# Performance work log

Hardware: AMD Instinct MI355X
Metric: run time of the kernel (lower is better)

## Reference

```python
import jax, jax.numpy as jnp
import numpy as np

EMBED_DIM = 2048
NUM_HEADS = 16
HEAD_DIM = EMBED_DIM // NUM_HEADS
WINDOW = 512          # sliding window size (inclusive: q - kv <= WINDOW)
CHUNK = WINDOW        # query chunk size; kv span per chunk = 2*CHUNK
SCALE = 1.0 / float(np.sqrt(HEAD_DIM))


def setup_inputs() -> dict:
    key = jax.random.key(0)
    k1, k2, k3 = jax.random.split(key, 3)
    B, S, E = 2, 4096, EMBED_DIM
    x = jax.random.normal(k1, (B, S, E), dtype=jnp.float32)
    # Linear weights, torch layout [out_features, in_features], small init for stability
    w_qkv = jax.random.normal(k2, (3 * E, E), dtype=jnp.float32) * (1.0 / np.sqrt(E))
    w_out = jax.random.normal(k3, (E, E), dtype=jnp.float32) * (1.0 / np.sqrt(E))
    return {"x": x, "w_qkv": w_qkv, "w_out": w_out}


def _sliding_window_attention(q, k, v):
    # q,k,v: [B,H,S,D]; causal + sliding-window (q_idx - kv_idx in [0, WINDOW])
    B, H, S, D = q.shape
    C = CHUNK
    nc = S // C
    qc = q.reshape(B, H, nc, C, D)                              # [B,H,nc,C,D]
    # pad one zero chunk in front of K/V so each query chunk sees (prev, cur)
    kp = jnp.pad(k, ((0, 0), (0, 0), (C, 0), (0, 0))).reshape(B, H, nc + 1, C, D)
    vp = jnp.pad(v, ((0, 0), (0, 0), (C, 0), (0, 0))).reshape(B, H, nc + 1, C, D)
    kc = jnp.concatenate([kp[:, :, :-1], kp[:, :, 1:]], axis=-2)  # [B,H,nc,2C,D]
    vc = jnp.concatenate([vp[:, :, :-1], vp[:, :, 1:]], axis=-2)  # [B,H,nc,2C,D]

    qa = jnp.arange(C)
    ka = jnp.arange(2 * C)
    diff = C + qa[:, None] - ka[None, :]                        # q_pos - kv_pos, [C,2C]
    base = (diff >= 0) & (diff <= WINDOW)                       # causal + window
    # mask out the zero-padding keys of the first chunk (global kv pos < 0)
    kv_pos = (jnp.arange(nc)[:, None] - 1) * C + ka[None, :]    # [nc,2C]
    mask = base[None, :, :] & (kv_pos >= 0)[:, None, :]         # [nc,C,2C]

    scores = jnp.einsum('bhncd,bhnkd->bhnck', qc, kc) * SCALE   # [B,H,nc,C,2C]
    scores = jnp.where(mask[None, None], scores, -jnp.inf)
    attn = jax.nn.softmax(scores, axis=-1)
    out = jnp.einsum('bhnck,bhnkd->bhncd', attn, vc)            # [B,H,nc,C,D]
    return out.reshape(B, H, S, D)


def reference(x, w_qkv, w_out):
    B, S, E = x.shape
    H, D = NUM_HEADS, HEAD_DIM
    qkv = x @ w_qkv.T                                           # [B,S,3E]
    qkv = qkv.reshape(B, S, 3, H, D).transpose(2, 0, 3, 1, 4)   # [3,B,H,S,D]
    q, k, v = qkv[0], qkv[1], qkv[2]
    o = _sliding_window_attention(q, k, v)                      # [B,H,S,D]
    o = o.transpose(0, 2, 1, 3).reshape(B, S, E)
    return o @ w_out.T
```

## Files before the change

### kernel.cpp

```cpp
#include <hip/hip_runtime.h>


typedef __bf16 bf16x8 __attribute__((ext_vector_type(8)));
typedef float  f32x4  __attribute__((ext_vector_type(4)));
typedef unsigned short u16x4 __attribute__((ext_vector_type(4)));

#define MFMA(a, b, c) __builtin_amdgcn_mfma_f32_16x16x32_bf16(a, b, c, 0, 0, 0)

__device__ __forceinline__ unsigned short f2bf(float f) {
  union { float f; unsigned u; } v; v.f = f;
  unsigned r = v.u + 0x7FFFu + ((v.u >> 16) & 1u);
  return (unsigned short)(r >> 16);
}

__device__ __forceinline__ void gl16(const void* g, void* l) {
  __builtin_amdgcn_global_load_lds(
      (const __attribute__((address_space(1))) unsigned int*)g,
      (__attribute__((address_space(3))) unsigned int*)l, 16, 0, 0);
}

__global__ void cast_bf16(const float4* __restrict__ in,
                          u16x4* __restrict__ out, int n4) {
  int i = blockIdx.x * blockDim.x + threadIdx.x;
  if (i < n4) {
    float4 v = in[i];
    u16x4 o;
    o[0] = f2bf(v.x); o[1] = f2bf(v.y); o[2] = f2bf(v.z); o[3] = f2bf(v.w);
    out[i] = o;
  }
}

template <int MODE>
__global__ __launch_bounds__(512, 2) void gemm_bt(
    const unsigned short* __restrict__ A, const unsigned short* __restrict__ Bw,
    void* __restrict__ C1, void* __restrict__ C2, int K, int Nstride) {
  __shared__ __align__(16) unsigned char sm[131072];
  const int tid = threadIdx.x, lane = tid & 63, w = tid >> 6;
  const int l15 = lane & 15, lg = lane >> 4;
  const int wr = w >> 2, wc = w & 3;

  int id = (int)blockIdx.x;
  int cpx = (int)gridDim.x >> 3;
  int sid = (id & 7) * cpx + (id >> 3);
  const int bm = (sid & 31) * 256;
  const int bn = (sid >> 5) * 256;

  f32x4 acc[8][4] = {};
  const int nt = K >> 6;

  const unsigned short* aRow0 = A  + (size_t)(bm + w * 16 + l15) * K + lg * 8;
  const unsigned short* aRow1 = A  + (size_t)(bm + (w + 8) * 16 + l15) * K + lg * 8;
  const unsigned short* bRow0 = Bw + (size_t)(bn + w * 16 + l15) * K + lg * 8;
  const unsigned short* bRow1 = Bw + (size_t)(bn + (w + 8) * 16 + l15) * K + lg * 8;

  auto stageA = [&](int t, int kk) {
    int kt = ((t < nt) ? t : nt - 1) * 64 + kk * 32;
    unsigned char* dst = sm + (t & 1) * 65536 + kk * 16384;
    gl16(aRow0 + kt, dst + w * 1024);
    gl16(aRow1 + kt, dst + (w + 8) * 1024);
  };
  auto stageB = [&](int t, int kk) {
    int kt = ((t < nt) ? t : nt - 1) * 64 + kk * 32;
    unsigned char* dst = sm + (t & 1) * 65536 + 32768 + kk * 16384;
    gl16(bRow0 + kt, dst + w * 1024);
    gl16(bRow1 + kt, dst + (w + 8) * 1024);
  };

  stageA(0, 0); stageB(0, 0);
  stageA(0, 1); stageB(0, 1);
  stageA(1, 0); stageB(1, 0);
  asm volatile("s_waitcnt vmcnt(8)" ::: "memory");
  __builtin_amdgcn_s_barrier();

#define PHASE(mh, kk, STAGE_STMT, DO_VM, READ_B)                               \
  {                                                                            \
    STAGE_STMT;                                                                \
    bf16x8 af[4];                                                              \
    _Pragma("unroll") for (int i = 0; i < 4; i++)                              \
      af[i] = *(const bf16x8*)(cur + ((kk)*16 + wr * 8 + (mh)*4 + i) * 1024 +  \
                               lane * 16);                                     \
    if (READ_B) {                                                              \
      _Pragma("unroll") for (int j = 0; j < 4; j++)                            \
        bfr[j] = *(const bf16x8*)(cur + 32768 +                                \
                                  ((kk)*16 + wc * 4 + j) * 1024 + lane * 16);  \
    }                                                                          \
    if (DO_VM) asm volatile("s_waitcnt vmcnt(8)" ::: "memory");                \
    __builtin_amdgcn_s_barrier();                                              \
    asm volatile("s_waitcnt lgkmcnt(0)" ::: "memory");                         \
    __builtin_amdgcn_sched_barrier(0);                                         \
    __builtin_amdgcn_s_setprio(1);                                             \
    _Pragma("unroll") for (int i = 0; i < 4; i++)                              \
      _Pragma("unroll") for (int j = 0; j < 4; j++)                            \
        acc[(mh)*4 + i][j] = MFMA(af[i], bfr[j], acc[(mh)*4 + i][j]);          \
    __builtin_amdgcn_s_setprio(0);                                             \
  }

  for (int g = 0; g < nt; ++g) {
    unsigned char* cur = sm + (g & 1) * 65536;
    bf16x8 bfr[4];
    PHASE(0, 0, , false, true)
    PHASE(1, 0, { stageA(g + 1, 1); stageB(g + 1, 1); }, true, false)
    PHASE(0, 1, , false, true)
    PHASE(1, 1, { stageA(g + 2, 0); stageB(g + 2, 0); }, true, false)
  }
#undef PHASE

  asm volatile("s_waitcnt vmcnt(0)" ::: "memory");

  if (MODE == 1) {
    unsigned short* QK = (unsigned short*)C1;
    unsigned short* VT = (unsigned short*)C2;
    if (bn < 4096) {
      const float scl = (bn < 2048) ? 0.08838834764831845f : 1.0f;
#pragma unroll
      for (int mi = 0; mi < 8; mi++) {
        int m0 = bm + wr * 128 + mi * 16 + lg * 4;
#pragma unroll
        for (int j = 0; j < 4; j++) {
          int n = bn + wc * 64 + j * 16 + l15;
#pragma unroll
          for (int r = 0; r < 4; r++)
            QK[(size_t)(m0 + r) * 4096 + n] = f2bf(acc[mi][j][r] * scl);
        }
      }
    } else {
#pragma unroll
      for (int mi = 0; mi < 8; mi++) {
        int m0 = bm + wr * 128 + mi * 16 + lg * 4;
        int bb = m0 >> 12, s = m0 & 4095;
#pragma unroll
        for (int j = 0; j < 4; j++) {
          int n4 = bn + wc * 64 + j * 16 + l15 - 4096;
          int hh = n4 >> 7, d = n4 & 127;
          u16x4 pk;
#pragma unroll
          for (int r = 0; r < 4; r++) pk[r] = f2bf(acc[mi][j][r]);
          *(u16x4*)(VT + ((size_t)((bb * 16 + hh) * 128 + d) * 4096 + s)) = pk;
        }
      }
    }
  } else {
    float* C = (float*)C1;
#pragma unroll
    for (int mi = 0; mi < 8; mi++) {
      int m0 = bm + wr * 128 + mi * 16 + lg * 4;
#pragma unroll
      for (int j = 0; j < 4; j++) {
        int n = bn + wc * 64 + j * 16 + l15;
#pragma unroll
        for (int r = 0; r < 4; r++)
          C[(size_t)(m0 + r) * Nstride + n] = acc[mi][j][r];
      }
    }
  }
}

__global__ __launch_bounds__(256, 2) void attn(
    const unsigned short* __restrict__ QK,
    const unsigned short* __restrict__ VT,
    unsigned short* __restrict__ O) {
  __shared__ unsigned char sm[51200];
  const int tid = threadIdx.x, lane = tid & 63, w = tid >> 6;
  const int l15 = lane & 15, lg = lane >> 4;
  const int bid = blockIdx.x;
  const int sid = (bid & 7) * 128 + (bid >> 3);
  const int qc = sid & 31, h = (sid >> 5) & 15, b = sid >> 9;
  const int q0 = qc * 128;

  bf16x8 qf[2][4];
#pragma unroll
  for (int mb = 0; mb < 2; mb++) {
    const unsigned short* qrow =
        QK + (size_t)(b * 4096 + q0 + (2 * w + mb) * 16 + l15) * 4096 + h * 128 + lg * 8;
#pragma unroll
    for (int ks = 0; ks < 4; ks++) qf[mb][ks] = *(const bf16x8*)(qrow + ks * 32);
  }

  float mrun[2] = {-1e30f, -1e30f}, lrun[2] = {0.f, 0.f};
  f32x4 oacc[8][2] = {};

  const int t0 = (q0 < 512) ? (512 - q0) >> 6 : 0;
  unsigned char* Ps = sm + 32768 + w * 4608;

  for (int t = t0; t < 10; t++) {
    const int kv0 = q0 - 512 + t * 64;
    __syncthreads();
#pragma unroll
    for (int u = 0; u < 4; u++) {
      int f = w + u * 4;
      int kvb = f >> 2, ks = f & 3;
      gl16(QK + (size_t)(b * 4096 + kv0 + kvb * 16 + l15) * 4096 + 2048 + h * 128 + ks * 32 + lg * 8,
           sm + (kvb * 4 + ks) * 1024);
      int db = f >> 1, kvs = f & 1;
      gl16(VT + (size_t)((b * 16 + h) * 128 + db * 16 + l15) * 4096 + kv0 + kvs * 32 + lg * 8,
           sm + 16384 + (db * 2 + kvs) * 1024);
    }
    __syncthreads();

    f32x4 sacc[4][2] = {};
#pragma unroll
    for (int ks = 0; ks < 4; ks++)
#pragma unroll
      for (int kvb = 0; kvb < 4; kvb++) {
        bf16x8 kf = *(const bf16x8*)(sm + (kvb * 4 + ks) * 1024 + lane * 16);
        sacc[kvb][0] = MFMA(kf, qf[0][ks], sacc[kvb][0]);
        sacc[kvb][1] = MFMA(kf, qf[1][ks], sacc[kvb][1]);
      }

    if (t <= 1 || t >= 8) {
#pragma unroll
      for (int kvb = 0; kvb < 4; kvb++)
#pragma unroll
        for (int mb = 0; mb < 2; mb++) {
          int qg = q0 + w * 32 + mb * 16 + l15;
          int kgb = kv0 + kvb * 16 + lg * 4;
#pragma unroll
          for (int r = 0; r < 4; r++) {
            int diff = qg - (kgb + r);
            if (diff < 0 || diff > 512) sacc[kvb][mb][r] = -1e30f;
          }
        }
    }

#pragma unroll
    for (int mb = 0; mb < 2; mb++) {
      float tmax = -1e30f;
#pragma unroll
      for (int kvb = 0; kvb < 4; kvb++)
#pragma unroll
        for (int r = 0; r < 4; r++) tmax = fmaxf(tmax, sacc[kvb][mb][r]);
      tmax = fmaxf(tmax, __shfl_xor(tmax, 16));
      tmax = fmaxf(tmax, __shfl_xor(tmax, 32));
      float mnew = fmaxf(mrun[mb], tmax);
      float alpha = __expf(mrun[mb] - mnew);
      mrun[mb] = mnew;
      float lsum = 0.f;
#pragma unroll
      for (int kvb = 0; kvb < 4; kvb++) {
        u16x4 pk;
#pragma unroll
        for (int r = 0; r < 4; r++) {
          float p = __expf(sacc[kvb][mb][r] - mnew);
          lsum += p;
          pk[r] = f2bf(p);
        }
        *(u16x4*)(Ps + (mb * 16 + l15) * 144 + kvb * 32 + lg * 8) = pk;
      }
      lsum += __shfl_xor(lsum, 16);
      lsum += __shfl_xor(lsum, 32);
      lrun[mb] = lrun[mb] * alpha + lsum;
#pragma unroll
      for (int db = 0; db < 8; db++)
#pragma unroll
        for (int r = 0; r < 4; r++) oacc[db][mb][r] *= alpha;
    }

#pragma unroll
    for (int kvs = 0; kvs < 2; kvs++) {
      bf16x8 pf0 = *(const bf16x8*)(Ps + (0 + l15) * 144 + kvs * 64 + lg * 16);
      bf16x8 pf1 = *(const bf16x8*)(Ps + (16 + l15) * 144 + kvs * 64 + lg * 16);
#pragma unroll
      for (int db = 0; db < 8; db++) {
        bf16x8 vf = *(const bf16x8*)(sm + 16384 + (db * 2 + kvs) * 1024 + lane * 16);
        oacc[db][0] = MFMA(vf, pf0, oacc[db][0]);
        oacc[db][1] = MFMA(vf, pf1, oacc[db][1]);
      }
    }
  }

#pragma unroll
  for (int mb = 0; mb < 2; mb++) {
    float inv = 1.0f / lrun[mb];
    int s = q0 + w * 32 + mb * 16 + l15;
    unsigned short* orow = O + (size_t)(b * 4096 + s) * 2048 + h * 128 + lg * 4;
#pragma unroll
    for (int db = 0; db < 8; db++) {
      u16x4 pk;
#pragma unroll
      for (int r = 0; r < 4; r++) pk[r] = f2bf(oacc[db][mb][r] * inv);
      *(u16x4*)(orow + db * 16) = pk;
    }
  }
}

extern "C" void kernel_launch(void* const* d_in, const int* in_sizes, int n_in,
                              void* d_out, int out_size, void* d_ws, size_t ws_size,
                              hipStream_t stream) {
  const float* x = (const float*)d_in[0];
  const float* w_qkv = (const float*)d_in[1];
  const float* w_out = (const float*)d_in[2];
  float* out = (float*)d_out;

  char* ws = (char*)d_ws;
  unsigned short* XB    = (unsigned short*)(ws);
  unsigned short* WQKVB = (unsigned short*)(ws + 33554432);
  unsigned short* WOUTB = (unsigned short*)(ws + 58720256);
  unsigned short* QKb   = (unsigned short*)(ws + 67108864);
  unsigned short* VTb   = (unsigned short*)(ws + 134217728);
  unsigned short* OB    = XB;

  cast_bf16<<<16384, 256, 0, stream>>>((const float4*)x, (u16x4*)XB, 4194304);
  cast_bf16<<<12288, 256, 0, stream>>>((const float4*)w_qkv, (u16x4*)WQKVB, 3145728);
  cast_bf16<<<4096, 256, 0, stream>>>((const float4*)w_out, (u16x4*)WOUTB, 1048576);

  gemm_bt<1><<<768, 512, 0, stream>>>(XB, WQKVB, QKb, VTb, 2048, 0);

  attn<<<1024, 256, 0, stream>>>(QKb, VTb, OB);

  gemm_bt<2><<<256, 512, 0, stream>>>(OB, WOUTB, out, nullptr, 2048, 2048);
}
```

Measured before the change: 536.1 us.

## Restructure GEMM to 4-stage K32 pipeline and prefetch K/V in attention

The GEMM main loop moves from a two-buffer, K=64 tile with four phases to a four-slot ring of K=32 tiles, issuing one stage per iteration three steps ahead. The attention kernel double-buffers the K tile and prefetches the next K and V tiles while the current tile is computed, replacing the two __syncthreads per iteration with vmcnt waits and barriers. Both changes aim to hide global-to-LDS load latency behind MFMA work. The cost is more LDS in attention (66 KB), which may limit occupancy, and more fine-grained barriers in the GEMM.

Result: no change. 527.7 us (-1.6%).

```diff
diff --git a/kernel.cpp b/kernel.cpp
--- a/kernel.cpp
+++ b/kernel.cpp
@@ -46,64 +46,61 @@
   const int bn = (sid >> 5) * 256;
 
   f32x4 acc[8][4] = {};
-  const int nt = K >> 6;
+  const int nt = K >> 5;
 
   const unsigned short* aRow0 = A  + (size_t)(bm + w * 16 + l15) * K + lg * 8;
   const unsigned short* aRow1 = A  + (size_t)(bm + (w + 8) * 16 + l15) * K + lg * 8;
   const unsigned short* bRow0 = Bw + (size_t)(bn + w * 16 + l15) * K + lg * 8;
   const unsigned short* bRow1 = Bw + (size_t)(bn + (w + 8) * 16 + l15) * K + lg * 8;
 
-  auto stageA = [&](int t, int kk) {
-    int kt = ((t < nt) ? t : nt - 1) * 64 + kk * 32;
-    unsigned char* dst = sm + (t & 1) * 65536 + kk * 16384;
+  auto stage = [&](int t) {
+    int kt = ((t < nt) ? t : nt - 1) * 32;
+    unsigned char* dst = sm + (t & 3) * 32768;
     gl16(aRow0 + kt, dst + w * 1024);
     gl16(aRow1 + kt, dst + (w + 8) * 1024);
+    gl16(bRow0 + kt, dst + 16384 + w * 1024);
+    gl16(bRow1 + kt, dst + 16384 + (w + 8) * 1024);
   };
-  auto stageB = [&](int t, int kk) {
-    int kt = ((t < nt) ? t : nt - 1) * 64 + kk * 32;
-    unsigned char* dst = sm + (t & 1) * 65536 + 32768 + kk * 16384;
-    gl16(bRow0 + kt, dst + w * 1024);
-    gl16(bRow1 + kt, dst + (w + 8) * 1024);
-  };
-
-  stageA(0, 0); stageB(0, 0);
-  stageA(0, 1); stageB(0, 1);
-  stageA(1, 0); stageB(1, 0);
+
+  stage(0); stage(1); stage(2);
   asm volatile("s_waitcnt vmcnt(8)" ::: "memory");
   __builtin_amdgcn_s_barrier();
 
-#define PHASE(mh, kk, STAGE_STMT, DO_VM, READ_B)                               \
-  {                                                                            \
-    STAGE_STMT;                                                                \
-    bf16x8 af[4];                                                              \
-    _Pragma("unroll") for (int i = 0; i < 4; i++)                              \
-      af[i] = *(const bf16x8*)(cur + ((kk)*16 + wr * 8 + (mh)*4 + i) * 1024 +  \
-                               lane * 16);                                     \
-    if (READ_B) {                                                              \
-      _Pragma("unroll") for (int j = 0; j < 4; j++)                            \
-        bfr[j] = *(const bf16x8*)(cur + 32768 +                                \
-                                  ((kk)*16 + wc * 4 + j) * 1024 + lane * 16);  \
-    }                                                                          \
-    if (DO_VM) asm volatile("s_waitcnt vmcnt(8)" ::: "memory");                \
-    __builtin_amdgcn_s_barrier();                                              \
-    asm volatile("s_waitcnt lgkmcnt(0)" ::: "memory");                         \
-    __builtin_amdgcn_sched_barrier(0);                                         \
-    __builtin_amdgcn_s_setprio(1);                                             \
-    _Pragma("unroll") for (int i = 0; i < 4; i++)                              \
-      _Pragma("unroll") for (int j = 0; j < 4; j++)                            \
-        acc[(mh)*4 + i][j] = MFMA(af[i], bfr[j], acc[(mh)*4 + i][j]);          \
-    __builtin_amdgcn_s_setprio(0);                                             \
-  }
-
   for (int g = 0; g < nt; ++g) {
-    unsigned char* cur = sm + (g & 1) * 65536;
-    bf16x8 bfr[4];
-    PHASE(0, 0, , false, true)
-    PHASE(1, 0, { stageA(g + 1, 1); stageB(g + 1, 1); }, true, false)
-    PHASE(0, 1, , false, true)
-    PHASE(1, 1, { stageA(g + 2, 0); stageB(g + 2, 0); }, true, false)
-  }
-#undef PHASE
+    unsigned char* cur = sm + (g & 3) * 32768;
+    bf16x8 af[4], bfr[4];
+#pragma unroll
+    for (int i = 0; i < 4; i++)
+      af[i] = *(const bf16x8*)(cur + (wr * 8 + i) * 1024 + lane * 16);
+#pragma unroll
+    for (int j = 0; j < 4; j++)
+      bfr[j] = *(const bf16x8*)(cur + 16384 + (wc * 4 + j) * 1024 + lane * 16);
+    __builtin_amdgcn_s_barrier();
+    asm volatile("s_waitcnt lgkmcnt(0)" ::: "memory");
+    __builtin_amdgcn_sched_barrier(0);
+    __builtin_amdgcn_s_setprio(1);
+#pragma unroll
+    for (int i = 0; i < 4; i++)
+#pragma unroll
+      for (int j = 0; j < 4; j++)
+        acc[i][j] = MFMA(af[i], bfr[j], acc[i][j]);
+    __builtin_amdgcn_s_setprio(0);
+#pragma unroll
+    for (int i = 0; i < 4; i++)
+      af[i] = *(const bf16x8*)(cur + (wr * 8 + 4 + i) * 1024 + lane * 16);
+    stage(g + 3);
+    asm volatile("s_waitcnt vmcnt(8)" ::: "memory");
+    __builtin_amdgcn_s_barrier();
+    asm volatile("s_waitcnt lgkmcnt(0)" ::: "memory");
+    __builtin_amdgcn_sched_barrier(0);
+    __builtin_amdgcn_s_setprio(1);
+#pragma unroll
+    for (int i = 0; i < 4; i++)
+#pragma unroll
+      for (int j = 0; j < 4; j++)
+        acc[4 + i][j] = MFMA(af[i], bfr[j], acc[4 + i][j]);
+    __builtin_amdgcn_s_setprio(0);
+  }
 
   asm volatile("s_waitcnt vmcnt(0)" ::: "memory");
 
@@ -159,7 +156,7 @@
     const unsigned short* __restrict__ QK,
     const unsigned short* __restrict__ VT,
     unsigned short* __restrict__ O) {
-  __shared__ unsigned char sm[51200];
+  __shared__ unsigned char sm[67584];
   const int tid = threadIdx.x, lane = tid & 63, w = tid >> 6;
   const int l15 = lane & 15, lg = lane >> 4;
   const int bid = blockIdx.x;
@@ -180,29 +177,44 @@
   f32x4 oacc[8][2] = {};
 
   const int t0 = (q0 < 512) ? (512 - q0) >> 6 : 0;
-  unsigned char* Ps = sm + 32768 + w * 4608;
-
-  for (int t = t0; t < 10; t++) {
-    const int kv0 = q0 - 512 + t * 64;
-    __syncthreads();
+  unsigned char* Ps = sm + 49152 + w * 4608;
+
+  {
+    const int kv0 = q0 - 512 + t0 * 64;
 #pragma unroll
     for (int u = 0; u < 4; u++) {
       int f = w + u * 4;
       int kvb = f >> 2, ks = f & 3;
       gl16(QK + (size_t)(b * 4096 + kv0 + kvb * 16 + l15) * 4096 + 2048 + h * 128 + ks * 32 + lg * 8,
-           sm + (kvb * 4 + ks) * 1024);
+           sm + (t0 & 1) * 16384 + f * 1024);
       int db = f >> 1, kvs = f & 1;
       gl16(VT + (size_t)((b * 16 + h) * 128 + db * 16 + l15) * 4096 + kv0 + kvs * 32 + lg * 8,
-           sm + 16384 + (db * 2 + kvs) * 1024);
-    }
-    __syncthreads();
+           sm + 32768 + f * 1024);
+    }
+  }
+  asm volatile("s_waitcnt vmcnt(0)" ::: "memory");
+  __builtin_amdgcn_s_barrier();
+
+  for (int t = t0; t < 10; t++) {
+    const int kv0 = q0 - 512 + t * 64;
+    const int X = t & 1;
+    const int tn = (t + 1 < 10) ? t + 1 : 9;
+    const int kvn = q0 - 512 + tn * 64;
+
+#pragma unroll
+    for (int u = 0; u < 4; u++) {
+      int f = w + u * 4;
+      int kvb = f >> 2, ks = f & 3;
+      gl16(QK + (size_t)(b * 4096 + kvn + kvb * 16 + l15) * 4096 + 2048 + h * 128 + ks * 32 + lg * 8,
+           sm + (X ^ 1) * 16384 + f * 1024);
+    }
 
     f32x4 sacc[4][2] = {};
 #pragma unroll
     for (int ks = 0; ks < 4; ks++)
 #pragma unroll
       for (int kvb = 0; kvb < 4; kvb++) {
-        bf16x8 kf = *(const bf16x8*)(sm + (kvb * 4 + ks) * 1024 + lane * 16);
+        bf16x8 kf = *(const bf16x8*)(sm + X * 16384 + (kvb * 4 + ks) * 1024 + lane * 16);
         sacc[kvb][0] = MFMA(kf, qf[0][ks], sacc[kvb][0]);
         sacc[kvb][1] = MFMA(kf, qf[1][ks], sacc[kvb][1]);
       }
@@ -255,18 +267,34 @@
         for (int r = 0; r < 4; r++) oacc[db][mb][r] *= alpha;
     }
 
+    asm volatile("s_waitcnt vmcnt(4)" ::: "memory");
+    __builtin_amdgcn_s_barrier();
+
 #pragma unroll
     for (int kvs = 0; kvs < 2; kvs++) {
       bf16x8 pf0 = *(const bf16x8*)(Ps + (0 + l15) * 144 + kvs * 64 + lg * 16);
       bf16x8 pf1 = *(const bf16x8*)(Ps + (16 + l15) * 144 + kvs * 64 + lg * 16);
 #pragma unroll
       for (int db = 0; db < 8; db++) {
-        bf16x8 vf = *(const bf16x8*)(sm + 16384 + (db * 2 + kvs) * 1024 + lane * 16);
+        bf16x8 vf = *(const bf16x8*)(sm + 32768 + (db * 2 + kvs) * 1024 + lane * 16);
         oacc[db][0] = MFMA(vf, pf0, oacc[db][0]);
         oacc[db][1] = MFMA(vf, pf1, oacc[db][1]);
       }
     }
-  }
+    __builtin_amdgcn_s_barrier();
+
+#pragma unroll
+    for (int u = 0; u < 4; u++) {
+      int f = w + u * 4;
+      int db = f >> 1, kvs = f & 1;
+      gl16(VT + (size_t)((b * 16 + h) * 128 + db * 16 + l15) * 4096 + kvn + kvs * 32 + lg * 8,
+           sm + 32768 + f * 1024);
+    }
+    asm volatile("s_waitcnt vmcnt(4)" ::: "memory");
+    __builtin_amdgcn_s_barrier();
+  }
+
+  asm volatile("s_waitcnt vmcnt(0)" ::: "memory");
 
 #pragma unroll
   for (int mb = 0; mb < 2; mb++) {
```
